# Optimization experiments

Hardware: AMD Instinct MI355X
Metric: run time of the kernel (lower is better)

The kernel has to match this reference:

```python
import jax, jax.numpy as jnp
import numpy as np

B, T, C = 8, 2048, 1024
CONTEXT_SIZE = T  # repo ties context_size to sequence length of the mask


def setup_inputs() -> dict:
    key = jax.random.key(0)
    ks = jax.random.split(key, 7)
    s = 1.0 / np.sqrt(C)
    return {
        "x": jax.random.normal(ks[0], (B, T, C), dtype=jnp.float32),
        "Wq": jax.random.normal(ks[1], (C, C), dtype=jnp.float32) * s,
        "bq": jax.random.normal(ks[2], (C,), dtype=jnp.float32) * s,
        "Wk": jax.random.normal(ks[3], (C, C), dtype=jnp.float32) * s,
        "bk": jax.random.normal(ks[4], (C,), dtype=jnp.float32) * s,
        "Wv": jax.random.normal(ks[5], (C, C), dtype=jnp.float32) * s,
        "bv": jax.random.normal(ks[6], (C,), dtype=jnp.float32) * s,
    }


def reference(x, Wq, bq, Wk, bk, Wv, bv):
    # x: [B, T, C]; weights stored as [in, out] so y = x @ W + b (same math as nn.Linear)
    Tlen = x.shape[1]
    q = x @ Wq + bq
    k = x @ Wk + bk
    v = x @ Wv + bv
    # NOTE: original scales by context_size**-0.5 (seq-length based), not head-dim
    scale = jnp.asarray(CONTEXT_SIZE, x.dtype) ** -0.5
    scores = jnp.einsum("btc,bsc->bts", q, k) * scale  # [B, T, T]
    causal = jnp.tril(jnp.ones((Tlen, Tlen), dtype=bool))
    scores = jnp.where(causal, scores, -jnp.inf)
    attn = jax.nn.softmax(scores, axis=-1)
    return jnp.einsum("bts,bsc->btc", attn, v)
```

## Files before the change

kernel.cpp:

```cpp
#include <hip/hip_runtime.h>

#define B_SZ 8
#define T_SZ 2048
#define C_SZ 1024

typedef __attribute__((ext_vector_type(8))) short short8;
typedef __attribute__((ext_vector_type(8))) unsigned short ushort8;
typedef __attribute__((ext_vector_type(4))) float f32x4;

__device__ __forceinline__ unsigned short f2bf(float x) {
  union { float f; unsigned u; } v; v.f = x;
  unsigned r = v.u + 0x7FFFu + ((v.u >> 16) & 1u);
  return (unsigned short)(r >> 16);
}
__device__ __forceinline__ float bf2f(unsigned short h) {
  union { unsigned u; float f; } v; v.u = ((unsigned)h) << 16;
  return v.f;
}

__device__ __forceinline__ void gload16(const void* g, void* l) {
  __builtin_amdgcn_global_load_lds(
      (const __attribute__((address_space(1))) unsigned int*)(uintptr_t)g,
      (__attribute__((address_space(3))) unsigned int*)(uintptr_t)l, 16, 0, 0);
}

__device__ __forceinline__ int xcd_swz(int orig, int nwg) {
  return (orig & 7) * (nwg >> 3) + (orig >> 3);
}

#define WAITV(N) asm volatile("s_waitcnt vmcnt(" #N ")" ::: "memory")
#define BAR1                            \
  {                                     \
    asm volatile("" ::: "memory");      \
    __builtin_amdgcn_s_barrier();       \
    __builtin_amdgcn_sched_barrier(0);  \
    asm volatile("" ::: "memory");      \
  }
#define BAR2                            \
  {                                     \
    asm volatile("" ::: "memory");      \
    __builtin_amdgcn_s_barrier();       \
    asm volatile("" ::: "memory");      \
  }

template <int LDA, int LDB>
__device__ __forceinline__ void nt8p(const unsigned short* __restrict__ Ab,
                                     const unsigned short* __restrict__ Bb,
                                     const int NT, unsigned short* lds,
                                     f32x4 (&acc)[2][4][4]) {
  const int lane = threadIdx.x & 63;
  const int wid = threadIdx.x >> 6;
  const int wr = wid >> 2;
  const int wc = wid & 3;
  const int fr = lane & 15;
  const int fq = lane >> 4;

  const int aslot = ((lane & 7) ^ (lane >> 3)) * 8;
  const int rr0 = (wid * 2 + 0) * 8 + (lane >> 3);
  const int rr1 = (wid * 2 + 1) * 8 + (lane >> 3);
  const unsigned short* pA0 =
      Ab + (size_t)((rr0 >> 6) * 128 + (rr0 & 63)) * LDA + aslot;
  const unsigned short* pA1 =
      Ab + (size_t)((rr1 >> 6) * 128 + (rr1 & 63)) * LDA + aslot;
  const int bslot = ((lane & 3) ^ ((lane >> 3) & 3)) * 8;
  const unsigned short* pB0 =
      Bb + (size_t)((wid * 2 + 0) * 16 + (lane >> 2)) * LDB + bslot;
  const unsigned short* pB1 =
      Bb + (size_t)((wid * 2 + 1) * 16 + (lane >> 2)) * LDB + bslot;
  const int ldsC0 = (wid * 2 + 0) * 512;
  const int ldsC1 = (wid * 2 + 1) * 512;

  const int arb = wr * 4096 + fr * 64;
  const int asw0 = ((0 * 4 + fq) ^ (fr & 7)) * 8;
  const int asw1 = ((1 * 4 + fq) ^ (fr & 7)) * 8;
  const int brb = 16384 + (wc * 64 + fr) * 32 + ((fq ^ ((fr >> 1) & 3)) * 8);

  short8 afq[4], afp[4], bf0[4], bf1[4];

#define STG_A(d, h, kt)                                           \
  {                                                               \
    gload16(pA0 + (size_t)(h) * 64 * LDA + (size_t)(kt) * 64,     \
            lds + (d) * 32768 + (h) * 8192 + ldsC0);              \
    gload16(pA1 + (size_t)(h) * 64 * LDA + (size_t)(kt) * 64,     \
            lds + (d) * 32768 + (h) * 8192 + ldsC1);              \
  }
#define STG_B(d, kh, kt)                                          \
  {                                                               \
    gload16(pB0 + (kh) * 32 + (size_t)(kt) * 64,                  \
            lds + (d) * 32768 + 16384 + (kh) * 8192 + ldsC0);     \
    gload16(pB1 + (kh) * 32 + (size_t)(kt) * 64,                  \
            lds + (d) * 32768 + 16384 + (kh) * 8192 + ldsC1);     \
  }
#define RD_A(dst, d, h, s)                                        \
  _Pragma("unroll") for (int mb = 0; mb < 4; ++mb) dst[mb] =      \
      *(const short8*)&lds[(d) * 32768 + (h) * 8192 + arb +       \
                           mb * 1024 + ((s) ? asw1 : asw0)];
#define RD_B(dst, d, s)                                           \
  _Pragma("unroll") for (int nb = 0; nb < 4; ++nb) dst[nb] =      \
      *(const short8*)&lds[(d) * 32768 + (s) * 8192 + brb + nb * 512];
#define MMQ(r, AF, BF)                                            \
  __builtin_amdgcn_s_setprio(1);                                  \
  _Pragma("unroll") for (int mb = 0; mb < 4; ++mb)                \
  _Pragma("unroll") for (int nb = 0; nb < 4; ++nb)                \
  acc[r][mb][nb] = __builtin_amdgcn_mfma_f32_16x16x32_bf16(       \
      AF[mb], BF[nb], acc[r][mb][nb], 0, 0, 0);                   \
  __builtin_amdgcn_s_setprio(0);

#define TILE_STEP(d, dn, TT)                                                  \
  {                                                                           \
    const int tp1 = ((TT) + 1 < NT) ? (TT) + 1 : NT - 1;                      \
    const int tp2 = ((TT) + 2 < NT) ? (TT) + 2 : NT - 1;                      \
                                                                      \
    RD_A(afp, d, 1, 0);                                                       \
    STG_B(dn, 1, tp1);                                                        \
    BAR1; MMQ(0, afq, bf0); BAR2;                                             \
                                                                      \
    WAITV(8);                                                                 \
    RD_A(afq, d, 0, 1); RD_B(bf1, d, 1);                                      \
    STG_A(dn, 1, tp1);                                                        \
    BAR1; MMQ(1, afp, bf0); BAR2;                                             \
                                                                      \
    WAITV(8);                                                                 \
    RD_A(afp, d, 1, 1);                                                       \
    STG_B(d, 0, tp2);                                                         \
    BAR1; MMQ(0, afq, bf1); BAR2;                                             \
                                                                      \
    WAITV(6);                                                                 \
    RD_A(afq, dn, 0, 0); RD_B(bf0, dn, 0);                                    \
    STG_A(d, 0, tp2);                                                         \
    BAR1; MMQ(1, afp, bf1); BAR2;                                             \
  }

  const int t1 = (NT > 1) ? 1 : 0;
  STG_A(0, 0, 0);
  STG_B(0, 0, 0);
  STG_B(0, 1, 0);
  STG_A(0, 1, 0);
  STG_B(1, 0, t1);
  STG_A(1, 0, t1);
  WAITV(8);
  BAR2;
  RD_A(afq, 0, 0, 0);
  RD_B(bf0, 0, 0);

  for (int T = 0; T < NT; T += 2) {
    TILE_STEP(0, 1, T);
    TILE_STEP(1, 0, T + 1);
  }
#undef STG_A
#undef STG_B
#undef RD_A
#undef RD_B
#undef MMQ
#undef TILE_STEP
}

__global__ __launch_bounds__(256) void convert_x(const float* __restrict__ x,
                                                 unsigned short* __restrict__ Xb,
                                                 int n8) {
  for (int i = blockIdx.x * blockDim.x + threadIdx.x; i < n8;
       i += gridDim.x * blockDim.x) {
    const float4* p = (const float4*)(x + (size_t)i * 8);
    float4 a = p[0], b = p[1];
    ushort8 u;
    u[0] = f2bf(a.x); u[1] = f2bf(a.y); u[2] = f2bf(a.z); u[3] = f2bf(a.w);
    u[4] = f2bf(b.x); u[5] = f2bf(b.y); u[6] = f2bf(b.z); u[7] = f2bf(b.w);
    *(ushort8*)(Xb + (size_t)i * 8) = u;
  }
}

__global__ __launch_bounds__(256) void transpose_w(
    const float* __restrict__ Wq, const float* __restrict__ Wk,
    const float* __restrict__ Wv, unsigned short* __restrict__ Wt) {
  const int z = blockIdx.z;
  const float* W = z == 0 ? Wq : (z == 1 ? Wk : Wv);
  unsigned short* O = Wt + (size_t)z * C_SZ * C_SZ;
  __shared__ float tl[32][33];
  const int bx = blockIdx.x * 32;
  const int by = blockIdx.y * 32;
  const int tx = threadIdx.x & 31;
  const int ty = threadIdx.x >> 5;
#pragma unroll
  for (int j = 0; j < 4; ++j)
    tl[ty + j * 8][tx] = W[(size_t)(by + ty + j * 8) * C_SZ + bx + tx];
  __syncthreads();
#pragma unroll
  for (int j = 0; j < 4; ++j)
    O[(size_t)(bx + ty + j * 8) * C_SZ + by + tx] = f2bf(tl[tx][ty + j * 8]);
}

__global__ __launch_bounds__(256) void transpose_v(
    const unsigned short* __restrict__ V, unsigned short* __restrict__ Vt) {
  const int b = blockIdx.z;
  __shared__ unsigned short tl[64][66];
  const int bx = blockIdx.x * 64;
  const int by = blockIdx.y * 64;
  const int tx = threadIdx.x & 63;
  const int ty = threadIdx.x >> 6;
  const unsigned short* Vb = V + (size_t)b * T_SZ * C_SZ;
  unsigned short* Ob = Vt + (size_t)b * C_SZ * T_SZ;
#pragma unroll
  for (int r = 0; r < 16; ++r)
    tl[ty * 16 + r][tx] = Vb[(size_t)(by + ty * 16 + r) * C_SZ + bx + tx];
  __syncthreads();
#pragma unroll
  for (int r = 0; r < 16; ++r)
    Ob[(size_t)(bx + ty * 16 + r) * T_SZ + by + tx] = tl[tx][ty * 16 + r];
}

__global__ __launch_bounds__(512, 2) void qkv_fused(
    const unsigned short* __restrict__ Xb, const unsigned short* __restrict__ Wt,
    const float* __restrict__ bq, const float* __restrict__ bk,
    const float* __restrict__ bv, unsigned short* __restrict__ QKV) {
  __shared__ unsigned short lds[65536] __attribute__((aligned(128)));
  const int wg = xcd_swz(blockIdx.x, 3 * 64 * 4);
  const int z = wg >> 8;
  const int rem = wg & 255;
  const int m0 = (rem >> 2) * 256;
  const int n0 = (rem & 3) * 256;
  const float* bias = z == 0 ? bq : (z == 1 ? bk : bv);

  f32x4 acc[2][4][4] = {};
  nt8p<C_SZ, C_SZ>(Xb + (size_t)m0 * C_SZ,
                   Wt + (size_t)z * C_SZ * C_SZ + (size_t)n0 * C_SZ,
                   C_SZ / 64, lds, acc);

  unsigned short* Y = QKV + (size_t)z * B_SZ * T_SZ * C_SZ;
  const int lane = threadIdx.x & 63;
  const int wid = threadIdx.x >> 6;
  const int wr = wid >> 2, wc = wid & 3;
  const int fr = lane & 15, fq = lane >> 4;
#pragma unroll
  for (int r = 0; r < 2; ++r)
#pragma unroll
    for (int nb = 0; nb < 4; ++nb) {
      const int col = n0 + wc * 64 + nb * 16 + fr;
      const float bvv = bias[col];
#pragma unroll
      for (int mb = 0; mb < 4; ++mb) {
        const int row0 = m0 + wr * 128 + r * 64 + mb * 16 + fq * 4;
#pragma unroll
        for (int j = 0; j < 4; ++j)
          Y[(size_t)(row0 + j) * C_SZ + col] = f2bf(acc[r][mb][nb][j] + bvv);
      }
    }
}

__global__ __launch_bounds__(512, 2) void scores_gemm(
    const unsigned short* __restrict__ Q, const unsigned short* __restrict__ Km,
    unsigned short* __restrict__ S, float scale) {
  const int wg = xcd_swz(blockIdx.x, B_SZ * 8 * 8);
  const int b = wg >> 6;
  const int rem = wg & 63;
  const int mt = rem >> 3, nt = rem & 7;
  if (nt > mt) return;
  const int m0 = mt * 256, n0 = nt * 256;
  __shared__ unsigned short lds[65536] __attribute__((aligned(128)));

  f32x4 acc[2][4][4] = {};
  nt8p<C_SZ, C_SZ>(Q + (size_t)b * T_SZ * C_SZ + (size_t)m0 * C_SZ,
                   Km + (size_t)b * T_SZ * C_SZ + (size_t)n0 * C_SZ,
                   C_SZ / 64, lds, acc);

  unsigned short* Sb = S + (size_t)b * T_SZ * T_SZ;
  const int lane = threadIdx.x & 63;
  const int wid = threadIdx.x >> 6;
  const int wr = wid >> 2, wc = wid & 3;
  const int fr = lane & 15, fq = lane >> 4;
#pragma unroll
  for (int r = 0; r < 2; ++r)
#pragma unroll
    for (int nb = 0; nb < 4; ++nb) {
      const int col = n0 + wc * 64 + nb * 16 + fr;
#pragma unroll
      for (int mb = 0; mb < 4; ++mb) {
        const int row0 = m0 + wr * 128 + r * 64 + mb * 16 + fq * 4;
#pragma unroll
        for (int j = 0; j < 4; ++j)
          Sb[(size_t)(row0 + j) * T_SZ + col] = f2bf(acc[r][mb][nb][j] * scale);
      }
    }
}

__device__ __forceinline__ float wredmax(float v) {
#pragma unroll
  for (int o = 32; o > 0; o >>= 1) v = fmaxf(v, __shfl_xor(v, o, 64));
  return v;
}
__device__ __forceinline__ float wredsum(float v) {
#pragma unroll
  for (int o = 32; o > 0; o >>= 1) v += __shfl_xor(v, o, 64);
  return v;
}

__global__ __launch_bounds__(256) void softmax_causal(
    unsigned short* __restrict__ S) {
  const int row = blockIdx.x;
  const int b = row >> 11;
  const int tq = row & (T_SZ - 1);
  unsigned short* sr = S + (size_t)b * T_SZ * T_SZ + (size_t)tq * T_SZ;
  const int len = tq + 1;
  const int wlen = (len + 255) & ~255;
  const int tid = threadIdx.x;
  const int lane = tid & 63;
  const int wid = tid >> 6;
  const int i0 = tid * 8;
  __shared__ float red[4];

  float v[8];
  float mx = -1e30f;
  if (i0 < len) {
    const ushort8 raw = *(const ushort8*)(sr + i0);
#pragma unroll
    for (int j = 0; j < 8; ++j) {
      v[j] = (i0 + j < len) ? bf2f(raw[j]) : -1e30f;
      mx = fmaxf(mx, v[j]);
    }
  } else {
#pragma unroll
    for (int j = 0; j < 8; ++j) v[j] = -1e30f;
  }
  mx = wredmax(mx);
  if (lane == 0) red[wid] = mx;
  __syncthreads();
  mx = fmaxf(fmaxf(red[0], red[1]), fmaxf(red[2], red[3]));
  __syncthreads();

  float sm = 0.f;
#pragma unroll
  for (int j = 0; j < 8; ++j) {
    v[j] = __expf(v[j] - mx);
    sm += v[j];
  }
  sm = wredsum(sm);
  if (lane == 0) red[wid] = sm;
  __syncthreads();
  sm = red[0] + red[1] + red[2] + red[3];
  const float inv = 1.f / sm;

  if (i0 < wlen) {
    ushort8 o;
#pragma unroll
    for (int j = 0; j < 8; ++j)
      o[j] = (i0 + j < len) ? f2bf(v[j] * inv) : (unsigned short)0;
    *(ushort8*)(sr + i0) = o;
  }
}

__global__ __launch_bounds__(512, 2) void pv_gemm(
    const unsigned short* __restrict__ P, const unsigned short* __restrict__ Vt,
    float* __restrict__ O) {
  const int wg = xcd_swz(blockIdx.x, B_SZ * 8 * 4);
  const int b = wg >> 5;
  const int rem = wg & 31;
  const int mt = rem >> 2, nt = rem & 3;
  const int m0 = mt * 256, n0 = nt * 256;
  __shared__ unsigned short lds[65536] __attribute__((aligned(128)));

  f32x4 acc[2][4][4] = {};
  nt8p<T_SZ, T_SZ>(P + (size_t)b * T_SZ * T_SZ + (size_t)m0 * T_SZ,
                   Vt + (size_t)b * C_SZ * T_SZ + (size_t)n0 * T_SZ,
                   4 * (mt + 1), lds, acc);

  float* Ob = O + (size_t)b * T_SZ * C_SZ;
  const int lane = threadIdx.x & 63;
  const int wid = threadIdx.x >> 6;
  const int wr = wid >> 2, wc = wid & 3;
  const int fr = lane & 15, fq = lane >> 4;
#pragma unroll
  for (int r = 0; r < 2; ++r)
#pragma unroll
    for (int nb = 0; nb < 4; ++nb) {
      const int col = n0 + wc * 64 + nb * 16 + fr;
#pragma unroll
      for (int mb = 0; mb < 4; ++mb) {
        const int row0 = m0 + wr * 128 + r * 64 + mb * 16 + fq * 4;
#pragma unroll
        for (int j = 0; j < 4; ++j)
          Ob[(size_t)(row0 + j) * C_SZ + col] = acc[r][mb][nb][j];
      }
    }
}

extern "C" void kernel_launch(void* const* d_in, const int* in_sizes, int n_in,
                              void* d_out, int out_size, void* d_ws,
                              size_t ws_size, hipStream_t stream) {
  (void)in_sizes; (void)n_in; (void)out_size; (void)ws_size;
  const float* x = (const float*)d_in[0];
  const float* Wq = (const float*)d_in[1];
  const float* bq = (const float*)d_in[2];
  const float* Wk = (const float*)d_in[3];
  const float* bk = (const float*)d_in[4];
  const float* Wv = (const float*)d_in[5];
  const float* bv = (const float*)d_in[6];
  float* out = (float*)d_out;

  const size_t TC = (size_t)B_SZ * T_SZ * C_SZ;
  unsigned short* Q = (unsigned short*)d_ws;
  unsigned short* K = Q + TC;
  unsigned short* V = K + TC;
  unsigned short* S = V + TC;
  unsigned short* Xb = S;
  unsigned short* Wt = S + TC;
  unsigned short* Vt = Q;

  const float scale = 0.022097086912079608f;

  hipLaunchKernelGGL(convert_x, dim3(2048), dim3(256), 0, stream, x, Xb,
                     (int)(TC / 8));
  hipLaunchKernelGGL(transpose_w, dim3(32, 32, 3), dim3(256), 0, stream, Wq,
                     Wk, Wv, Wt);
  hipLaunchKernelGGL(qkv_fused, dim3(3 * 64 * 4), dim3(512), 0, stream, Xb, Wt,
                     bq, bk, bv, Q);
  hipLaunchKernelGGL(scores_gemm, dim3(B_SZ * 8 * 8), dim3(512), 0, stream, Q,
                     K, S, scale);
  hipLaunchKernelGGL(transpose_v, dim3(16, 32, 8), dim3(256), 0, stream, V,
                     Vt);
  hipLaunchKernelGGL(softmax_causal, dim3(B_SZ * T_SZ), dim3(256), 0, stream,
                     S);
  hipLaunchKernelGGL(pv_gemm, dim3(B_SZ * 8 * 4), dim3(512), 0, stream, S, Vt,
                     out);
}
```

Baseline: 268.8 us.

## Stage GEMM epilogues through LDS and write V transposed directly

All three GEMM epilogues now spill each wave's accumulator fragment into a per-wave LDS scratch tile and read it back row-wise, so global stores become 16-byte vector writes instead of scattered 2/4-byte writes. The QKV projection writes V already transposed into the Vt buffer, which removes the separate transpose_v kernel and its extra round trip through global memory. In exchange each epilogue adds an LDS round trip and a full barrier after the main loop. Vt now gets its own workspace slot instead of aliasing Q.

```diff
diff --git a/kernel.cpp b/kernel.cpp
--- a/kernel.cpp
+++ b/kernel.cpp
@@ -155,6 +155,13 @@
 #undef TILE_STEP
 }
 
+#define EPI_DUMP(r, mh)                                               \
+  _Pragma("unroll") for (int mb2 = 0; mb2 < 2; ++mb2)                 \
+  _Pragma("unroll") for (int nb = 0; nb < 4; ++nb)                    \
+  _Pragma("unroll") for (int j = 0; j < 4; ++j)                       \
+      ldw[(mb2 * 16 + fq * 4 + j) * 66 + nb * 16 + fr] =              \
+          acc[r][(mh) * 2 + mb2][nb][j];
+
 __global__ __launch_bounds__(256) void convert_x(const float* __restrict__ x,
                                                  unsigned short* __restrict__ Xb,
                                                  int n8) {
@@ -189,61 +196,83 @@
     O[(size_t)(bx + ty + j * 8) * C_SZ + by + tx] = f2bf(tl[tx][ty + j * 8]);
 }
 
-__global__ __launch_bounds__(256) void transpose_v(
-    const unsigned short* __restrict__ V, unsigned short* __restrict__ Vt) {
-  const int b = blockIdx.z;
-  __shared__ unsigned short tl[64][66];
-  const int bx = blockIdx.x * 64;
-  const int by = blockIdx.y * 64;
-  const int tx = threadIdx.x & 63;
-  const int ty = threadIdx.x >> 6;
-  const unsigned short* Vb = V + (size_t)b * T_SZ * C_SZ;
-  unsigned short* Ob = Vt + (size_t)b * C_SZ * T_SZ;
-#pragma unroll
-  for (int r = 0; r < 16; ++r)
-    tl[ty * 16 + r][tx] = Vb[(size_t)(by + ty * 16 + r) * C_SZ + bx + tx];
-  __syncthreads();
-#pragma unroll
-  for (int r = 0; r < 16; ++r)
-    Ob[(size_t)(bx + ty * 16 + r) * T_SZ + by + tx] = tl[tx][ty * 16 + r];
-}
-
 __global__ __launch_bounds__(512, 2) void qkv_fused(
     const unsigned short* __restrict__ Xb, const unsigned short* __restrict__ Wt,
     const float* __restrict__ bq, const float* __restrict__ bk,
-    const float* __restrict__ bv, unsigned short* __restrict__ QKV) {
+    const float* __restrict__ bv, unsigned short* __restrict__ Q,
+    unsigned short* __restrict__ K, unsigned short* __restrict__ Vt) {
   __shared__ unsigned short lds[65536] __attribute__((aligned(128)));
   const int wg = xcd_swz(blockIdx.x, 3 * 64 * 4);
   const int z = wg >> 8;
   const int rem = wg & 255;
   const int m0 = (rem >> 2) * 256;
   const int n0 = (rem & 3) * 256;
-  const float* bias = z == 0 ? bq : (z == 1 ? bk : bv);
 
   f32x4 acc[2][4][4] = {};
   nt8p<C_SZ, C_SZ>(Xb + (size_t)m0 * C_SZ,
                    Wt + (size_t)z * C_SZ * C_SZ + (size_t)n0 * C_SZ,
                    C_SZ / 64, lds, acc);
 
-  unsigned short* Y = QKV + (size_t)z * B_SZ * T_SZ * C_SZ;
   const int lane = threadIdx.x & 63;
   const int wid = threadIdx.x >> 6;
   const int wr = wid >> 2, wc = wid & 3;
   const int fr = lane & 15, fq = lane >> 4;
-#pragma unroll
-  for (int r = 0; r < 2; ++r)
-#pragma unroll
-    for (int nb = 0; nb < 4; ++nb) {
-      const int col = n0 + wc * 64 + nb * 16 + fr;
-      const float bvv = bias[col];
-#pragma unroll
-      for (int mb = 0; mb < 4; ++mb) {
-        const int row0 = m0 + wr * 128 + r * 64 + mb * 16 + fq * 4;
-#pragma unroll
-        for (int j = 0; j < 4; ++j)
-          Y[(size_t)(row0 + j) * C_SZ + col] = f2bf(acc[r][mb][nb][j] + bvv);
+
+  WAITV(0);
+  __syncthreads();
+  float* ldw = (float*)lds + wid * 2112;
+
+  if (z < 2) {
+    unsigned short* Y = (z == 0) ? Q : K;
+    const float* bias = (z == 0) ? bq : bk;
+    const int cbase = n0 + wc * 64 + (lane & 7) * 8;
+    float bb[8];
+#pragma unroll
+    for (int k = 0; k < 8; ++k) bb[k] = bias[cbase + k];
+#pragma unroll
+    for (int r = 0; r < 2; ++r)
+#pragma unroll
+      for (int mh = 0; mh < 2; ++mh) {
+        EPI_DUMP(r, mh);
+        const int rbase = m0 + wr * 128 + r * 64 + mh * 32;
+#pragma unroll
+        for (int i = 0; i < 4; ++i) {
+          const int rl = i * 8 + (lane >> 3);
+          const f32x4 lo = *(const f32x4*)&ldw[rl * 66 + (lane & 7) * 8];
+          const f32x4 hi = *(const f32x4*)&ldw[rl * 66 + (lane & 7) * 8 + 4];
+          ushort8 o;
+#pragma unroll
+          for (int k = 0; k < 4; ++k) o[k] = f2bf(lo[k] + bb[k]);
+#pragma unroll
+          for (int k = 0; k < 4; ++k) o[4 + k] = f2bf(hi[k] + bb[4 + k]);
+          *(ushort8*)&Y[(size_t)(rbase + rl) * C_SZ + cbase] = o;
+        }
       }
-    }
+  } else {
+    const int b2 = m0 >> 11;
+    const int tb = m0 & (T_SZ - 1);
+    unsigned short* Vtb = Vt + (size_t)b2 * C_SZ * T_SZ;
+    const int cb = n0 + wc * 64;
+    float bv4[4];
+#pragma unroll
+    for (int i = 0; i < 4; ++i) bv4[i] = bv[cb + (lane >> 2) + i * 16];
+#pragma unroll
+    for (int r = 0; r < 2; ++r)
+#pragma unroll
+      for (int mh = 0; mh < 2; ++mh) {
+        EPI_DUMP(r, mh);
+        const int t0 = tb + wr * 128 + r * 64 + mh * 32 + (lane & 3) * 8;
+#pragma unroll
+        for (int i = 0; i < 4; ++i) {
+          const int c = (lane >> 2) + i * 16;
+          ushort8 o;
+#pragma unroll
+          for (int k = 0; k < 8; ++k)
+            o[k] = f2bf(ldw[((lane & 3) * 8 + k) * 66 + c] + bv4[i]);
+          *(ushort8*)&Vtb[(size_t)(cb + c) * T_SZ + t0] = o;
+        }
+      }
+  }
 }
 
 __global__ __launch_bounds__(512, 2) void scores_gemm(
@@ -267,17 +296,28 @@
   const int wid = threadIdx.x >> 6;
   const int wr = wid >> 2, wc = wid & 3;
   const int fr = lane & 15, fq = lane >> 4;
+
+  WAITV(0);
+  __syncthreads();
+  float* ldw = (float*)lds + wid * 2112;
+  const int cbase = n0 + wc * 64 + (lane & 7) * 8;
 #pragma unroll
   for (int r = 0; r < 2; ++r)
 #pragma unroll
-    for (int nb = 0; nb < 4; ++nb) {
-      const int col = n0 + wc * 64 + nb * 16 + fr;
-#pragma unroll
-      for (int mb = 0; mb < 4; ++mb) {
-        const int row0 = m0 + wr * 128 + r * 64 + mb * 16 + fq * 4;
-#pragma unroll
-        for (int j = 0; j < 4; ++j)
-          Sb[(size_t)(row0 + j) * T_SZ + col] = f2bf(acc[r][mb][nb][j] * scale);
+    for (int mh = 0; mh < 2; ++mh) {
+      EPI_DUMP(r, mh);
+      const int rbase = m0 + wr * 128 + r * 64 + mh * 32;
+#pragma unroll
+      for (int i = 0; i < 4; ++i) {
+        const int rl = i * 8 + (lane >> 3);
+        const f32x4 lo = *(const f32x4*)&ldw[rl * 66 + (lane & 7) * 8];
+        const f32x4 hi = *(const f32x4*)&ldw[rl * 66 + (lane & 7) * 8 + 4];
+        ushort8 o;
+#pragma unroll
+        for (int k = 0; k < 4; ++k) o[k] = f2bf(lo[k] * scale);
+#pragma unroll
+        for (int k = 0; k < 4; ++k) o[4 + k] = f2bf(hi[k] * scale);
+        *(ushort8*)&Sb[(size_t)(rbase + rl) * T_SZ + cbase] = o;
       }
     }
 }
@@ -367,17 +407,22 @@
   const int wid = threadIdx.x >> 6;
   const int wr = wid >> 2, wc = wid & 3;
   const int fr = lane & 15, fq = lane >> 4;
+
+  WAITV(0);
+  __syncthreads();
+  float* ldw = (float*)lds + wid * 2112;
+  const int cbase = n0 + wc * 64 + (lane & 15) * 4;
 #pragma unroll
   for (int r = 0; r < 2; ++r)
 #pragma unroll
-    for (int nb = 0; nb < 4; ++nb) {
-      const int col = n0 + wc * 64 + nb * 16 + fr;
-#pragma unroll
-      for (int mb = 0; mb < 4; ++mb) {
-        const int row0 = m0 + wr * 128 + r * 64 + mb * 16 + fq * 4;
-#pragma unroll
-        for (int j = 0; j < 4; ++j)
-          Ob[(size_t)(row0 + j) * C_SZ + col] = acc[r][mb][nb][j];
+    for (int mh = 0; mh < 2; ++mh) {
+      EPI_DUMP(r, mh);
+      const int rbase = m0 + wr * 128 + r * 64 + mh * 32;
+#pragma unroll
+      for (int i = 0; i < 8; ++i) {
+        const int rl = i * 4 + (lane >> 4);
+        const f32x4 v = *(const f32x4*)&ldw[rl * 66 + (lane & 15) * 4];
+        *(f32x4*)&Ob[(size_t)(rbase + rl) * C_SZ + cbase] = v;
       }
     }
 }
@@ -398,11 +443,10 @@
   const size_t TC = (size_t)B_SZ * T_SZ * C_SZ;
   unsigned short* Q = (unsigned short*)d_ws;
   unsigned short* K = Q + TC;
-  unsigned short* V = K + TC;
-  unsigned short* S = V + TC;
+  unsigned short* Vt = K + TC;
+  unsigned short* S = Vt + TC;
   unsigned short* Xb = S;
   unsigned short* Wt = S + TC;
-  unsigned short* Vt = Q;
 
   const float scale = 0.022097086912079608f;
 
@@ -411,11 +455,9 @@
   hipLaunchKernelGGL(transpose_w, dim3(32, 32, 3), dim3(256), 0, stream, Wq,
                      Wk, Wv, Wt);
   hipLaunchKernelGGL(qkv_fused, dim3(3 * 64 * 4), dim3(512), 0, stream, Xb, Wt,
-                     bq, bk, bv, Q);
+                     bq, bk, bv, Q, K, Vt);
   hipLaunchKernelGGL(scores_gemm, dim3(B_SZ * 8 * 8), dim3(512), 0, stream, Q,
                      K, S, scale);
-  hipLaunchKernelGGL(transpose_v, dim3(16, 32, 8), dim3(256), 0, stream, V,
-                     Vt);
   hipLaunchKernelGGL(softmax_causal, dim3(B_SZ * T_SZ), dim3(256), 0, stream,
                      S);
   hipLaunchKernelGGL(pv_gemm, dim3(B_SZ * 8 * 4), dim3(512), 0, stream, S, Vt,
```

Result: slower. 279.5 us (+4.0%).
